# Optimization experiments

Measured on AMD Instinct MI355X. Metric: run time of the kernel, lower is better.

The kernel has to match this reference:

```python
import jax, jax.numpy as jnp
import numpy as np

B = 131072      # batch
G = 8           # number of groups
GS = 8          # features per group (n_features = G*GS = 64)
K = 8           # n_basis
O = 16          # kan_out_dim
TOT = G * O     # 128, GroupKANLayer output dim
R = 10          # n_rules
FIN = 20        # fuzzy_in_dim = max(2*n_rules, 8)
EPS_BN = 1e-5


def setup_inputs() -> dict:
    key = jax.random.key(0)
    ks = jax.random.split(key, 8)
    x = jax.random.normal(ks[0], (B, G * GS), dtype=jnp.float32)
    # per-group GaussianRBF params (one shared RBF per group, applied to each feature)
    rbf_centres = jnp.tile(jnp.linspace(-3.0, 3.0, K, dtype=jnp.float32)[None, :], (G, 1))
    rbf_log_widths = jnp.zeros((G, K), dtype=jnp.float32)
    rbf_weights = jax.random.normal(ks[1], (G, K), dtype=jnp.float32) * 0.1
    rbf_linear_w = jnp.ones((G,), dtype=jnp.float32)
    # group projections: kaiming normal fan_in (relu gain sqrt(2))
    proj_W = jax.random.normal(ks[2], (G, O, GS), dtype=jnp.float32) * np.sqrt(2.0 / GS)
    proj_b = jnp.zeros((G, O), dtype=jnp.float32)
    bn1_gamma = jnp.ones((TOT,), dtype=jnp.float32)
    bn1_beta = jnp.zeros((TOT,), dtype=jnp.float32)
    # fuzzy_proj linear (xavier uniform) TOT -> FIN
    a = np.sqrt(6.0 / (TOT + FIN))
    fp_W = jax.random.uniform(ks[3], (FIN, TOT), dtype=jnp.float32, minval=-a, maxval=a)
    fp_b = jnp.zeros((FIN,), dtype=jnp.float32)
    bn2_gamma = jnp.ones((FIN,), dtype=jnp.float32)
    bn2_beta = jnp.zeros((FIN,), dtype=jnp.float32)
    # IT2 fuzzy layer params
    fz_centres = jax.random.uniform(ks[4], (R, FIN), dtype=jnp.float32, minval=-1.0, maxval=1.0)
    fz_log_su = jnp.full((R, FIN), -0.7, dtype=jnp.float32)
    fz_log_sl = jnp.full((R, FIN), -1.2, dtype=jnp.float32)
    # sparse rule head
    head_W = jax.random.normal(ks[5], (1, R), dtype=jnp.float32) * 0.05
    head_b = jnp.zeros((1,), dtype=jnp.float32)
    return {
        'x': x, 'rbf_centres': rbf_centres, 'rbf_log_widths': rbf_log_widths,
        'rbf_weights': rbf_weights, 'rbf_linear_w': rbf_linear_w,
        'proj_W': proj_W, 'proj_b': proj_b,
        'bn1_gamma': bn1_gamma, 'bn1_beta': bn1_beta,
        'fp_W': fp_W, 'fp_b': fp_b, 'bn2_gamma': bn2_gamma, 'bn2_beta': bn2_beta,
        'fz_centres': fz_centres, 'fz_log_su': fz_log_su, 'fz_log_sl': fz_log_sl,
        'head_W': head_W, 'head_b': head_b,
    }


def _batchnorm(h, gamma, beta):
    # training-mode BatchNorm1d: normalize with batch mean / biased variance
    mu = h.mean(axis=0)
    var = h.var(axis=0)
    return (h - mu) * jax.lax.rsqrt(var + EPS_BN) * gamma + beta


def _forward(x, rbf_centres, rbf_log_widths, rbf_weights, rbf_linear_w,
             proj_W, proj_b, bn1_gamma, bn1_beta, fp_W, fp_b,
             bn2_gamma, bn2_beta, fz_centres, fz_log_su, fz_log_sl,
             head_W, head_b):
    b = x.shape[0]
    xg = x.reshape(b, G, GS)                               # groups are contiguous index slices
    sigma = jnp.exp(rbf_log_widths) + 1e-6                 # [G,K]
    # Gaussian RBF over all groups/features at once: [B,G,GS,K]
    rbf = jnp.exp(-0.5 * ((xg[..., None] - rbf_centres[:, None, :]) / sigma[:, None, :]) ** 2)
    act = rbf_linear_w[None, :, None] * xg + jnp.einsum('bgfk,gk->bgf', rbf, rbf_weights)
    proj = jnp.einsum('bgf,gof->bgo', act, proj_W) + proj_b  # grouped linear, [B,G,O]
    h = _batchnorm(proj.reshape(b, TOT), bn1_gamma, bn1_beta)
    # fuzzy_proj: Linear -> BN -> GELU (torch default GELU = exact erf form)
    z = _batchnorm(h @ fp_W.T + fp_b, bn2_gamma, bn2_beta)
    z = jax.nn.gelu(z, approximate=False)                    # [B,FIN]
    # IT2 fuzzy memberships
    su = jnp.exp(fz_log_su) + 1e-6                           # [R,FIN]
    sl = jnp.minimum(jnp.exp(fz_log_sl) + 1e-6, su * 0.9)
    diff = z[:, None, :] - fz_centres[None]                  # [B,R,FIN]
    upper = jnp.exp(-0.5 * (diff / su[None]) ** 2).mean(-1)  # [B,R]
    lower = jnp.exp(-0.5 * (diff / sl[None]) ** 2).mean(-1)
    firing = 0.5 * (upper + lower)
    return firing @ head_W.T + head_b                        # [B,1]


def reference(x, rbf_centres, rbf_log_widths, rbf_weights, rbf_linear_w,
              proj_W, proj_b, bn1_gamma, bn1_beta, fp_W, fp_b,
              bn2_gamma, bn2_beta, fz_centres, fz_log_su, fz_log_sl,
              head_W, head_b):
    return _forward(x, rbf_centres, rbf_log_widths, rbf_weights, rbf_linear_w,
                    proj_W, proj_b, bn1_gamma, bn1_beta, fp_W, fp_b,
                    bn2_gamma, bn2_beta, fz_centres, fz_log_su, fz_log_sl,
                    head_W, head_b)
```

## Files before the change

### kernel.cpp

```cpp
#include <hip/hip_runtime.h>
#include <hip/hip_fp16.h>
#include <math.h>

#define B_N 131072

#define WS_STAT1 0
#define ST1_SZ   (64 * 352)
#define WS_MT    22528
#define WS_C     23808
#define WS_STAT2 23840
#define WS_NH    26400
#define WS_ACTH  26816
#define WS_Z     (26816 + (size_t)B_N * 32)
#define WS_END   (WS_Z + (size_t)B_N * 20)

struct alignas(16) H8 { __half2 a, b, c, d; };

__device__ __forceinline__ float gelu_exact(float v) {
    return 0.5f * v * (1.0f + erff(v * 0.70710678118654752440f));
}

__global__ __launch_bounds__(256) void k_act_moments(
    const float* __restrict__ x, const float* __restrict__ cen,
    const float* __restrict__ lw, const float* __restrict__ rw,
    const float* __restrict__ linw, __half* __restrict__ act_h,
    float* __restrict__ stat1, int store)
{
    __shared__ float sAcc[4][8][44];
    const int t = threadIdx.x;
    const int g = t & 7;
    const int rl = t >> 3;

    float c_[8], nh_[8], w_[8];
#pragma unroll
    for (int k = 0; k < 8; ++k) {
        c_[k] = cen[g * 8 + k];
        float s = expf(lw[g * 8 + k]) + 1e-6f;
        nh_[k] = -0.5f / (s * s);
        w_[k] = rw[g * 8 + k];
    }
    const float lin = linw[g];
    const float c0 = c_[0], nh0 = nh_[0];
    const float delta = c_[1] - c_[0];

    bool uni = true;
#pragma unroll
    for (int k = 0; k < 8; ++k) {
        float ck = c0 + (float)k * delta;
        uni = uni && (fabsf(c_[k] - ck) <= 1e-5f * (1.0f + fabsf(ck)));
        uni = uni && (fabsf(nh_[k] - nh0) <= 1e-6f * fabsf(nh0));
    }
    const bool fast = (bool)__all((int)uni);

    float W_[8];
    float k1 = 0.0f;
    if (fast) {
        k1 = -2.0f * delta * nh0;
#pragma unroll
        for (int k = 0; k < 8; ++k) {
            float kd = (float)k * delta;
            W_[k] = w_[k] * __expf(nh0 * kd * kd);
        }
    }

    float sumA[8], P[36];
#pragma unroll
    for (int f = 0; f < 8; ++f) sumA[f] = 0.0f;
#pragma unroll
    for (int i = 0; i < 36; ++i) P[i] = 0.0f;

    if (fast) {
#pragma unroll 1
        for (int row = blockIdx.x * 32 + rl; row < B_N; row += gridDim.x * 32) {
            const float* xr = x + (size_t)row * 64 + g * 8;
            float4 v0 = *(const float4*)(xr);
            float4 v1 = *(const float4*)(xr + 4);
            float xv[8] = {v0.x, v0.y, v0.z, v0.w, v1.x, v1.y, v1.z, v1.w};
            float act[8];
#pragma unroll
            for (int f = 0; f < 8; ++f) {
                float v = xv[f];
                float dv = v - c0;
                float E0 = __expf(nh0 * dv * dv);
                float T  = __expf(k1 * dv);
                float poly = W_[7];
#pragma unroll
                for (int k = 6; k >= 0; --k) poly = poly * T + W_[k];
                act[f] = lin * v + E0 * poly;
            }
            if (store) {
                H8 h;
                h.a = __floats2half2_rn(act[0], act[1]);
                h.b = __floats2half2_rn(act[2], act[3]);
                h.c = __floats2half2_rn(act[4], act[5]);
                h.d = __floats2half2_rn(act[6], act[7]);
                *(H8*)(act_h + (size_t)row * 64 + g * 8) = h;
            }
            int idx = 0;
#pragma unroll
            for (int f = 0; f < 8; ++f) {
                sumA[f] += act[f];
#pragma unroll
                for (int f2 = 0; f2 <= f; ++f2) { P[idx] += act[f] * act[f2]; ++idx; }
            }
        }
    } else {
#pragma unroll 1
        for (int row = blockIdx.x * 32 + rl; row < B_N; row += gridDim.x * 32) {
            const float* xr = x + (size_t)row * 64 + g * 8;
            float4 v0 = *(const float4*)(xr);
            float4 v1 = *(const float4*)(xr + 4);
            float xv[8] = {v0.x, v0.y, v0.z, v0.w, v1.x, v1.y, v1.z, v1.w};
            float act[8];
#pragma unroll
            for (int f = 0; f < 8; ++f) {
                float v = xv[f];
                float a = lin * v;
#pragma unroll
                for (int k = 0; k < 8; ++k) {
                    float d = v - c_[k];
                    a += w_[k] * __expf(d * d * nh_[k]);
                }
                act[f] = a;
            }
            if (store) {
                H8 h;
                h.a = __floats2half2_rn(act[0], act[1]);
                h.b = __floats2half2_rn(act[2], act[3]);
                h.c = __floats2half2_rn(act[4], act[5]);
                h.d = __floats2half2_rn(act[6], act[7]);
                *(H8*)(act_h + (size_t)row * 64 + g * 8) = h;
            }
            int idx = 0;
#pragma unroll
            for (int f = 0; f < 8; ++f) {
                sumA[f] += act[f];
#pragma unroll
                for (int f2 = 0; f2 <= f; ++f2) { P[idx] += act[f] * act[f2]; ++idx; }
            }
        }
    }

#pragma unroll
    for (int off = 32; off >= 8; off >>= 1) {
#pragma unroll
        for (int f = 0; f < 8; ++f) sumA[f] += __shfl_down(sumA[f], off, 64);
#pragma unroll
        for (int i = 0; i < 36; ++i) P[i] += __shfl_down(P[i], off, 64);
    }
    const int wave = t >> 6, lane = t & 63;
    if (lane < 8) {
        float* dst = &sAcc[wave][lane][0];
#pragma unroll
        for (int f = 0; f < 8; ++f) dst[f] = sumA[f];
#pragma unroll
        for (int i = 0; i < 36; ++i) dst[8 + i] = P[i];
    }
    __syncthreads();
    for (int i = t; i < 352; i += 256) {
        int gg = i / 44, v = i % 44;
        float s = sAcc[0][gg][v] + sAcc[1][gg][v] + sAcc[2][gg][v] + sAcc[3][gg][v];
        atomicAdd(&stat1[(blockIdx.x & 63) * 352 + i], s);
    }
}

__global__ __launch_bounds__(256) void k_build(
    const float* __restrict__ stat1, const float* __restrict__ fpW,
    const float* __restrict__ fpb, const float* __restrict__ g1,
    const float* __restrict__ b1, const float* __restrict__ Wp,
    const float* __restrict__ pb, const float* __restrict__ lsu,
    const float* __restrict__ lsl,
    float* __restrict__ Mt, float* __restrict__ Cc, float* __restrict__ nh,
    float* __restrict__ stat2)
{
    __shared__ float Am[8][8];
    __shared__ float Sg[8][36];
    __shared__ float a_[128], bb_[128];
    const int t = threadIdx.x;
    for (int i = t; i < 352; i += 256) {
        float s = 0.0f;
        for (int st = 0; st < 64; ++st) s += stat1[st * 352 + i];
        float m = s * (1.0f / B_N);
        int g = i / 44, v = i % 44;
        if (v < 8) Am[g][v] = m; else Sg[g][v - 8] = m;
    }
    __syncthreads();
    if (t < 128) {
        const int g = t >> 4;
        float wv[8];
#pragma unroll
        for (int f = 0; f < 8; ++f) wv[f] = Wp[t * 8 + f];
        float dot = 0.0f;
#pragma unroll
        for (int f = 0; f < 8; ++f) dot += wv[f] * Am[g][f];
        const float pbv = pb[t];
        const float mu = pbv + dot;
        float e2 = pbv * pbv + 2.0f * pbv * dot;
        int idx = 0;
#pragma unroll
        for (int f = 0; f < 8; ++f)
#pragma unroll
            for (int f2 = 0; f2 <= f; ++f2) {
                float c2 = (f2 == f) ? 1.0f : 2.0f;
                e2 += c2 * wv[f] * wv[f2] * Sg[g][idx]; ++idx;
            }
        const float var = fmaxf(e2 - mu * mu, 0.0f);
        const float a = g1[t] * rsqrtf(var + 1e-5f);
        a_[t] = a;
        bb_[t] = b1[t] - mu * a;
    }
    __syncthreads();
    for (int i = t; i < 1280; i += 256) {
        int gf = i / 20, j = i % 20;
        int g = gf >> 3, f = gf & 7;
        float m = 0.0f;
        for (int o = 0; o < 16; ++o) {
            int c = g * 16 + o;
            m += fpW[j * 128 + c] * a_[c] * Wp[c * 8 + f];
        }
        Mt[i] = m;
    }
    if (t < 20) {
        float cj = fpb[t];
        for (int c = 0; c < 128; ++c)
            cj += fpW[t * 128 + c] * (a_[c] * pb[c] + bb_[c]);
        Cc[t] = cj;
    }
    for (int i = t; i < 200; i += 256) {
        float su = expf(lsu[i]) + 1e-6f;
        float sl = fminf(expf(lsl[i]) + 1e-6f, 0.9f * su);
        nh[i] = -0.5f / (su * su);
        nh[200 + i] = -0.5f / (sl * sl);
    }
    for (int i = t; i < 2560; i += 256) stat2[i] = 0.0f;
}

__global__ __launch_bounds__(256) void k_z(
    const __half* __restrict__ act_h, const float* __restrict__ Mt,
    const float* __restrict__ Cc, float* __restrict__ zout,
    float* __restrict__ stat2)
{
    __shared__ float sRed[4][40];
    const int t = threadIdx.x;
    const int row = blockIdx.x * 256 + t;

    float zp[20];
#pragma unroll
    for (int j = 0; j < 20; ++j) zp[j] = Cc[j];

#pragma unroll 1
    for (int g = 0; g < 8; ++g) {
        const H8 h = *(const H8*)(act_h + (size_t)row * 64 + g * 8);
        float2 f0 = __half22float2(h.a), f1 = __half22float2(h.b);
        float2 f2 = __half22float2(h.c), f3 = __half22float2(h.d);
        float a[8] = {f0.x, f0.y, f1.x, f1.y, f2.x, f2.y, f3.x, f3.y};
#pragma unroll
        for (int f = 0; f < 8; ++f) {
            const float* m = Mt + (g * 8 + f) * 20;
            float av = a[f];
#pragma unroll
            for (int j = 0; j < 20; ++j) zp[j] += av * m[j];
        }
    }

#pragma unroll
    for (int j = 0; j < 20; ++j) zout[(size_t)j * B_N + row] = zp[j];

    float s_[20], q_[20];
#pragma unroll
    for (int j = 0; j < 20; ++j) { s_[j] = zp[j]; q_[j] = zp[j] * zp[j]; }
#pragma unroll
    for (int off = 32; off >= 1; off >>= 1) {
#pragma unroll
        for (int j = 0; j < 20; ++j) {
            s_[j] += __shfl_down(s_[j], off, 64);
            q_[j] += __shfl_down(q_[j], off, 64);
        }
    }
    const int wave = t >> 6, lane = t & 63;
    if (lane == 0) {
#pragma unroll
        for (int j = 0; j < 20; ++j) { sRed[wave][j] = s_[j]; sRed[wave][20 + j] = q_[j]; }
    }
    __syncthreads();
    if (t < 40) {
        float v = sRed[0][t] + sRed[1][t] + sRed[2][t] + sRed[3][t];
        atomicAdd(&stat2[(blockIdx.x & 63) * 40 + t], v);
    }
}

__global__ __launch_bounds__(256) void k_zpre_stats(
    const float* __restrict__ x, const float* __restrict__ cen,
    const float* __restrict__ lw, const float* __restrict__ rw,
    const float* __restrict__ linw, const float* __restrict__ Mt,
    const float* __restrict__ Cc, float* __restrict__ zout,
    float* __restrict__ stat2)
{
    __shared__ __align__(16) float4 sRbf[64];
    __shared__ float sLin[8], sC[20];
    __shared__ __align__(16) float sMt[1280];
    __shared__ float sRed[4][40];
    const int t = threadIdx.x;
    if (t < 64) {
        float s = expf(lw[t]) + 1e-6f;
        sRbf[t] = make_float4(cen[t], rw[t], -0.5f / (s * s), 0.0f);
    }
    if (t < 8)  sLin[t] = linw[t];
    if (t < 20) sC[t] = Cc[t];
    for (int i = t; i < 1280; i += 256) sMt[i] = Mt[i];
    __syncthreads();
    const int row = blockIdx.x * 256 + t;
    const float* xr = x + (size_t)row * 64;
    float zp[20];
#pragma unroll
    for (int j = 0; j < 20; ++j) zp[j] = sC[j];
#pragma unroll 1
    for (int g = 0; g < 8; ++g) {
        float4 v0 = *(const float4*)(xr + g * 8);
        float4 v1 = *(const float4*)(xr + g * 8 + 4);
        float xv[8] = {v0.x, v0.y, v0.z, v0.w, v1.x, v1.y, v1.z, v1.w};
        float act[8];
        float lin = sLin[g];
#pragma unroll
        for (int f = 0; f < 8; ++f) act[f] = lin * xv[f];
#pragma unroll 1
        for (int k = 0; k < 8; ++k) {
            float4 p = sRbf[g * 8 + k];
#pragma unroll
            for (int f = 0; f < 8; ++f) {
                float d = xv[f] - p.x;
                act[f] += p.y * __expf(d * d * p.z);
            }
        }
#pragma unroll 1
        for (int f = 0; f < 8; ++f) {
            float av = act[f];
            const float4* m4 = (const float4*)(sMt + (g * 8 + f) * 20);
            float4 ma = m4[0], mb = m4[1], mc = m4[2], md = m4[3], me = m4[4];
            zp[0] += av * ma.x; zp[1] += av * ma.y; zp[2] += av * ma.z; zp[3] += av * ma.w;
            zp[4] += av * mb.x; zp[5] += av * mb.y; zp[6] += av * mb.z; zp[7] += av * mb.w;
            zp[8] += av * mc.x; zp[9] += av * mc.y; zp[10] += av * mc.z; zp[11] += av * mc.w;
            zp[12] += av * md.x; zp[13] += av * md.y; zp[14] += av * md.z; zp[15] += av * md.w;
            zp[16] += av * me.x; zp[17] += av * me.y; zp[18] += av * me.z; zp[19] += av * me.w;
        }
    }
#pragma unroll
    for (int j = 0; j < 20; ++j) zout[(size_t)j * B_N + row] = zp[j];
    float s_[20], q_[20];
#pragma unroll
    for (int j = 0; j < 20; ++j) { s_[j] = zp[j]; q_[j] = zp[j] * zp[j]; }
#pragma unroll
    for (int off = 32; off >= 1; off >>= 1) {
#pragma unroll
        for (int j = 0; j < 20; ++j) {
            s_[j] += __shfl_down(s_[j], off, 64);
            q_[j] += __shfl_down(q_[j], off, 64);
        }
    }
    const int wave = t >> 6, lane = t & 63;
    if (lane == 0) {
#pragma unroll
        for (int j = 0; j < 20; ++j) { sRed[wave][j] = s_[j]; sRed[wave][20 + j] = q_[j]; }
    }
    __syncthreads();
    if (t < 40) {
        float v = sRed[0][t] + sRed[1][t] + sRed[2][t] + sRed[3][t];
        atomicAdd(&stat2[(blockIdx.x & 63) * 40 + t], v);
    }
}

__global__ __launch_bounds__(256) void k_out(
    const float* __restrict__ zin, const float* __restrict__ stat2,
    const float* __restrict__ g2, const float* __restrict__ b2,
    const float* __restrict__ nh, const float* __restrict__ fzc,
    const float* __restrict__ hW, const float* __restrict__ hb,
    float* __restrict__ out)
{
    __shared__ float sT[40], sSc[20], sSh[20];
    const int t = threadIdx.x;
    if (t < 40) {
        float s = 0.0f;
        for (int st = 0; st < 64; ++st) s += stat2[st * 40 + t];
        sT[t] = s;
    }
    __syncthreads();
    if (t < 20) {
        float mu = sT[t] * (1.0f / B_N);
        float var = fmaxf(sT[20 + t] * (1.0f / B_N) - mu * mu, 0.0f);
        float sc = g2[t] * rsqrtf(var + 1e-5f);
        sSc[t] = sc;
        sSh[t] = b2[t] - mu * sc;
    }
    __syncthreads();

    const int row = blockIdx.x * 256 + t;
    float z[20];
#pragma unroll
    for (int j = 0; j < 20; ++j) {
        float v = zin[(size_t)j * B_N + row];
        z[j] = gelu_exact(sSc[j] * v + sSh[j]);
    }
    float acc = hb[0];
#pragma unroll 1
    for (int r = 0; r < 10; ++r) {
        float u = 0.0f, l = 0.0f;
#pragma unroll
        for (int j = 0; j < 20; ++j) {
            float cx = fzc[r * 20 + j];
            float pu = nh[r * 20 + j];
            float pl = nh[200 + r * 20 + j];
            float d = z[j] - cx;
            float dd = d * d;
            u += __expf(dd * pu);
            l += __expf(dd * pl);
        }
        acc += hW[r] * 0.025f * (u + l);
    }
    out[row] = acc;
}

extern "C" void kernel_launch(void* const* d_in, const int* in_sizes, int n_in,
                              void* d_out, int out_size, void* d_ws, size_t ws_size,
                              hipStream_t stream) {
    const float* x    = (const float*)d_in[0];
    const float* cen  = (const float*)d_in[1];
    const float* lw   = (const float*)d_in[2];
    const float* rw   = (const float*)d_in[3];
    const float* linw = (const float*)d_in[4];
    const float* Wp   = (const float*)d_in[5];
    const float* pb   = (const float*)d_in[6];
    const float* g1   = (const float*)d_in[7];
    const float* b1   = (const float*)d_in[8];
    const float* fpW  = (const float*)d_in[9];
    const float* fpb  = (const float*)d_in[10];
    const float* g2   = (const float*)d_in[11];
    const float* b2   = (const float*)d_in[12];
    const float* fzc  = (const float*)d_in[13];
    const float* lsu  = (const float*)d_in[14];
    const float* lsl  = (const float*)d_in[15];
    const float* hW   = (const float*)d_in[16];
    const float* hb   = (const float*)d_in[17];

    float* ws    = (float*)d_ws;
    float* stat1 = ws + WS_STAT1;
    float* Mt    = ws + WS_MT;
    float* Cc    = ws + WS_C;
    float* stat2 = ws + WS_STAT2;
    float* nh    = ws + WS_NH;
    __half* acth = (__half*)(ws + WS_ACTH);
    float* zbuf  = ws + WS_Z;
    float* outp  = (float*)d_out;

    const size_t needFull = WS_END * sizeof(float);
    const int mode = (ws_size >= needFull) ? 2 : 1;
    if (mode == 1) zbuf = ws + WS_ACTH;

    hipMemsetAsync(stat1, 0, (size_t)ST1_SZ * sizeof(float), stream);
    k_act_moments<<<1024, 256, 0, stream>>>(x, cen, lw, rw, linw, acth, stat1,
                                            mode == 2 ? 1 : 0);
    k_build<<<1, 256, 0, stream>>>(stat1, fpW, fpb, g1, b1, Wp, pb, lsu, lsl,
                                   Mt, Cc, nh, stat2);
    if (mode == 2) {
        k_z<<<512, 256, 0, stream>>>(acth, Mt, Cc, zbuf, stat2);
    } else {
        k_zpre_stats<<<512, 256, 0, stream>>>(x, cen, lw, rw, linw, Mt, Cc,
                                              zbuf, stat2);
    }
    k_out<<<512, 256, 0, stream>>>(zbuf, stat2, g2, b2, nh, fzc, hW, hb, outp);
}
```

Measured before the change: 162.2 us.

## Compute full 64x64 activation Gram to derive BN2 stats analytically, drop z pass

The stats kernel now accumulates the full 64x64 second-moment matrix of the RBF activations through a shared-memory tiled outer product, instead of only per-group moments. The build kernel uses it to compute the second batchnorm's mean and variance in closed form and folds the BN2 scale and shift into the projection matrix. That removes the intermediate z/activation buffers and the separate z-statistics kernel. The final kernel recomputes activations from x and applies GELU plus the fuzzy head directly, trading one full pass of reads and writes for extra atomics and a heavier single-block build step.

```diff
diff --git a/kernel.cpp b/kernel.cpp
--- a/kernel.cpp
+++ b/kernel.cpp
@@ -1,35 +1,32 @@
 #include <hip/hip_runtime.h>
-#include <hip/hip_fp16.h>
 #include <math.h>
 
 #define B_N 131072
-
-#define WS_STAT1 0
-#define ST1_SZ   (64 * 352)
-#define WS_MT    22528
-#define WS_C     23808
-#define WS_STAT2 23840
-#define WS_NH    26400
-#define WS_ACTH  26816
-#define WS_Z     (26816 + (size_t)B_N * 32)
-#define WS_END   (WS_Z + (size_t)B_N * 20)
-
-struct alignas(16) H8 { __half2 a, b, c, d; };
+#define NSTRIPE 16
+#define ST_STRIDE 4160
+#define WS_STAT 0
+#define ST_SZ   (NSTRIPE * ST_STRIDE)
+#define WS_MT2  66560
+#define WS_C2   67840
+#define WS_NH   67860
+#define WS_FT   68260
 
 __device__ __forceinline__ float gelu_exact(float v) {
     return 0.5f * v * (1.0f + erff(v * 0.70710678118654752440f));
 }
 
-__global__ __launch_bounds__(256) void k_act_moments(
+__global__ __launch_bounds__(256, 2) void k_stats(
     const float* __restrict__ x, const float* __restrict__ cen,
     const float* __restrict__ lw, const float* __restrict__ rw,
-    const float* __restrict__ linw, __half* __restrict__ act_h,
-    float* __restrict__ stat1, int store)
+    const float* __restrict__ linw, float* __restrict__ stat)
 {
-    __shared__ float sAcc[4][8][44];
-    const int t = threadIdx.x;
-    const int g = t & 7;
+    __shared__ float sAct[2][32][64];
+    __shared__ float sAcc[4][8][8];
+    const int t  = threadIdx.x;
+    const int g  = t & 7;
     const int rl = t >> 3;
+    const int gi = t >> 4;
+    const int gj = t & 15;
 
     float c_[8], nh_[8], w_[8];
 #pragma unroll
@@ -53,9 +50,9 @@
     const bool fast = (bool)__all((int)uni);
 
     float W_[8];
-    float k1 = 0.0f;
+    float k1c = 0.0f;
     if (fast) {
-        k1 = -2.0f * delta * nh0;
+        k1c = -2.0f * delta * nh0;
 #pragma unroll
         for (int k = 0; k < 8; ++k) {
             float kd = (float)k * delta;
@@ -63,55 +60,46 @@
         }
     }
 
-    float sumA[8], P[36];
+    float sumA[8];
 #pragma unroll
     for (int f = 0; f < 8; ++f) sumA[f] = 0.0f;
-#pragma unroll
-    for (int i = 0; i < 36; ++i) P[i] = 0.0f;
-
-    if (fast) {
+    float Ga[4][4];
+#pragma unroll
+    for (int a = 0; a < 4; ++a)
+#pragma unroll
+        for (int b = 0; b < 4; ++b) Ga[a][b] = 0.0f;
+
+    float4 pv0, pv1;
+    {
+        const float* xr = x + ((size_t)(blockIdx.x * 32 + rl)) * 64 + g * 8;
+        pv0 = *(const float4*)xr;
+        pv1 = *(const float4*)(xr + 4);
+    }
+
+    int p = 0;
 #pragma unroll 1
-        for (int row = blockIdx.x * 32 + rl; row < B_N; row += gridDim.x * 32) {
-            const float* xr = x + (size_t)row * 64 + g * 8;
-            float4 v0 = *(const float4*)(xr);
-            float4 v1 = *(const float4*)(xr + 4);
-            float xv[8] = {v0.x, v0.y, v0.z, v0.w, v1.x, v1.y, v1.z, v1.w};
-            float act[8];
+    for (int c = 0; c < 8; ++c) {
+        float xv[8] = {pv0.x, pv0.y, pv0.z, pv0.w, pv1.x, pv1.y, pv1.z, pv1.w};
+        if (c < 7) {
+            const float* xr =
+                x + ((size_t)(blockIdx.x * 32 + (c + 1) * 16384 + rl)) * 64 + g * 8;
+            pv0 = *(const float4*)xr;
+            pv1 = *(const float4*)(xr + 4);
+        }
+        float act[8];
+        if (fast) {
 #pragma unroll
             for (int f = 0; f < 8; ++f) {
                 float v = xv[f];
                 float dv = v - c0;
                 float E0 = __expf(nh0 * dv * dv);
-                float T  = __expf(k1 * dv);
+                float T  = __expf(k1c * dv);
                 float poly = W_[7];
 #pragma unroll
                 for (int k = 6; k >= 0; --k) poly = poly * T + W_[k];
                 act[f] = lin * v + E0 * poly;
             }
-            if (store) {
-                H8 h;
-                h.a = __floats2half2_rn(act[0], act[1]);
-                h.b = __floats2half2_rn(act[2], act[3]);
-                h.c = __floats2half2_rn(act[4], act[5]);
-                h.d = __floats2half2_rn(act[6], act[7]);
-                *(H8*)(act_h + (size_t)row * 64 + g * 8) = h;
-            }
-            int idx = 0;
-#pragma unroll
-            for (int f = 0; f < 8; ++f) {
-                sumA[f] += act[f];
-#pragma unroll
-                for (int f2 = 0; f2 <= f; ++f2) { P[idx] += act[f] * act[f2]; ++idx; }
-            }
-        }
-    } else {
-#pragma unroll 1
-        for (int row = blockIdx.x * 32 + rl; row < B_N; row += gridDim.x * 32) {
-            const float* xr = x + (size_t)row * 64 + g * 8;
-            float4 v0 = *(const float4*)(xr);
-            float4 v1 = *(const float4*)(xr + 4);
-            float xv[8] = {v0.x, v0.y, v0.z, v0.w, v1.x, v1.y, v1.z, v1.w};
-            float act[8];
+        } else {
 #pragma unroll
             for (int f = 0; f < 8; ++f) {
                 float v = xv[f];
@@ -123,68 +111,84 @@
                 }
                 act[f] = a;
             }
-            if (store) {
-                H8 h;
-                h.a = __floats2half2_rn(act[0], act[1]);
-                h.b = __floats2half2_rn(act[2], act[3]);
-                h.c = __floats2half2_rn(act[4], act[5]);
-                h.d = __floats2half2_rn(act[6], act[7]);
-                *(H8*)(act_h + (size_t)row * 64 + g * 8) = h;
-            }
-            int idx = 0;
-#pragma unroll
-            for (int f = 0; f < 8; ++f) {
-                sumA[f] += act[f];
-#pragma unroll
-                for (int f2 = 0; f2 <= f; ++f2) { P[idx] += act[f] * act[f2]; ++idx; }
-            }
-        }
-    }
-
-#pragma unroll
-    for (int off = 32; off >= 8; off >>= 1) {
+        }
+#pragma unroll
+        for (int f = 0; f < 8; ++f) sumA[f] += act[f];
+        *(float4*)&sAct[p][rl][g * 8]     = make_float4(act[0], act[1], act[2], act[3]);
+        *(float4*)&sAct[p][rl][g * 8 + 4] = make_float4(act[4], act[5], act[6], act[7]);
+        __syncthreads();
+        const float (*buf)[64] = sAct[p];
+#pragma unroll
+        for (int r = 0; r < 32; ++r) {
+            const float4 va = *(const float4*)&buf[r][gi * 4];
+            const float4 vb = *(const float4*)&buf[r][gj * 4];
+            Ga[0][0] += va.x * vb.x; Ga[0][1] += va.x * vb.y;
+            Ga[0][2] += va.x * vb.z; Ga[0][3] += va.x * vb.w;
+            Ga[1][0] += va.y * vb.x; Ga[1][1] += va.y * vb.y;
+            Ga[1][2] += va.y * vb.z; Ga[1][3] += va.y * vb.w;
+            Ga[2][0] += va.z * vb.x; Ga[2][1] += va.z * vb.y;
+            Ga[2][2] += va.z * vb.z; Ga[2][3] += va.z * vb.w;
+            Ga[3][0] += va.w * vb.x; Ga[3][1] += va.w * vb.y;
+            Ga[3][2] += va.w * vb.z; Ga[3][3] += va.w * vb.w;
+        }
+        p ^= 1;
+    }
+
+#pragma unroll
+    for (int off = 32; off >= 8; off >>= 1)
 #pragma unroll
         for (int f = 0; f < 8; ++f) sumA[f] += __shfl_down(sumA[f], off, 64);
-#pragma unroll
-        for (int i = 0; i < 36; ++i) P[i] += __shfl_down(P[i], off, 64);
-    }
     const int wave = t >> 6, lane = t & 63;
     if (lane < 8) {
-        float* dst = &sAcc[wave][lane][0];
-#pragma unroll
-        for (int f = 0; f < 8; ++f) dst[f] = sumA[f];
-#pragma unroll
-        for (int i = 0; i < 36; ++i) dst[8 + i] = P[i];
-    }
-    __syncthreads();
-    for (int i = t; i < 352; i += 256) {
-        int gg = i / 44, v = i % 44;
-        float s = sAcc[0][gg][v] + sAcc[1][gg][v] + sAcc[2][gg][v] + sAcc[3][gg][v];
-        atomicAdd(&stat1[(blockIdx.x & 63) * 352 + i], s);
-    }
+#pragma unroll
+        for (int f = 0; f < 8; ++f) sAcc[wave][lane][f] = sumA[f];
+    }
+    __syncthreads();
+    const int stripe = (blockIdx.x & (NSTRIPE - 1)) * ST_STRIDE;
+    if (t < 64) {
+        int gg = t >> 3, f = t & 7;
+        float s = sAcc[0][gg][f] + sAcc[1][gg][f] + sAcc[2][gg][f] + sAcc[3][gg][f];
+        atomicAdd(&stat[stripe + t], s);
+    }
+#pragma unroll
+    for (int a = 0; a < 4; ++a)
+#pragma unroll
+        for (int b = 0; b < 4; ++b)
+            atomicAdd(&stat[stripe + 64 + (gi * 4 + a) * 64 + (gj * 4 + b)], Ga[a][b]);
 }
 
 __global__ __launch_bounds__(256) void k_build(
-    const float* __restrict__ stat1, const float* __restrict__ fpW,
-    const float* __restrict__ fpb, const float* __restrict__ g1,
-    const float* __restrict__ b1, const float* __restrict__ Wp,
-    const float* __restrict__ pb, const float* __restrict__ lsu,
-    const float* __restrict__ lsl,
-    float* __restrict__ Mt, float* __restrict__ Cc, float* __restrict__ nh,
-    float* __restrict__ stat2)
+    const float* __restrict__ stat, const float* __restrict__ Wp,
+    const float* __restrict__ pb, const float* __restrict__ g1,
+    const float* __restrict__ b1, const float* __restrict__ fpW,
+    const float* __restrict__ fpb, const float* __restrict__ g2,
+    const float* __restrict__ b2, const float* __restrict__ lsu,
+    const float* __restrict__ lsl, const float* __restrict__ cen,
+    const float* __restrict__ lw, const float* __restrict__ rw,
+    const float* __restrict__ linw,
+    float* __restrict__ Mt2, float* __restrict__ C2,
+    float* __restrict__ nh, float* __restrict__ ftab)
 {
-    __shared__ float Am[8][8];
-    __shared__ float Sg[8][36];
-    __shared__ float a_[128], bb_[128];
+    __shared__ float sG[4096];
+    __shared__ float sAm[64];
+    __shared__ float sa[128], sbb[128];
+    __shared__ float sMt[1280];
+    __shared__ float sC[20];
+    __shared__ float sQ[20][8];
+    __shared__ float sDM[20];
+    __shared__ float sSc[20];
+    __shared__ int   sUni[8];
     const int t = threadIdx.x;
-    for (int i = t; i < 352; i += 256) {
+    const float invB = 1.0f / (float)B_N;
+
+    for (int i = t; i < ST_STRIDE; i += 256) {
         float s = 0.0f;
-        for (int st = 0; st < 64; ++st) s += stat1[st * 352 + i];
-        float m = s * (1.0f / B_N);
-        int g = i / 44, v = i % 44;
-        if (v < 8) Am[g][v] = m; else Sg[g][v - 8] = m;
-    }
-    __syncthreads();
+        for (int st = 0; st < NSTRIPE; ++st) s += stat[st * ST_STRIDE + i];
+        if (i < 64) sAm[i] = s * invB;
+        else        sG[i - 64] = s;
+    }
+    __syncthreads();
+
     if (t < 128) {
         const int g = t >> 4;
         float wv[8];
@@ -192,144 +196,190 @@
         for (int f = 0; f < 8; ++f) wv[f] = Wp[t * 8 + f];
         float dot = 0.0f;
 #pragma unroll
-        for (int f = 0; f < 8; ++f) dot += wv[f] * Am[g][f];
+        for (int f = 0; f < 8; ++f) dot += wv[f] * sAm[g * 8 + f];
         const float pbv = pb[t];
         const float mu = pbv + dot;
-        float e2 = pbv * pbv + 2.0f * pbv * dot;
-        int idx = 0;
-#pragma unroll
-        for (int f = 0; f < 8; ++f)
-#pragma unroll
-            for (int f2 = 0; f2 <= f; ++f2) {
-                float c2 = (f2 == f) ? 1.0f : 2.0f;
-                e2 += c2 * wv[f] * wv[f2] * Sg[g][idx]; ++idx;
-            }
-        const float var = fmaxf(e2 - mu * mu, 0.0f);
-        const float a = g1[t] * rsqrtf(var + 1e-5f);
-        a_[t] = a;
-        bb_[t] = b1[t] - mu * a;
-    }
-    __syncthreads();
+        float q = 0.0f;
+#pragma unroll
+        for (int f = 0; f < 8; ++f) {
+            float inner = 0.0f;
+#pragma unroll
+            for (int f2 = 0; f2 < 8; ++f2)
+                inner += wv[f2] * sG[(g * 8 + f) * 64 + (g * 8 + f2)];
+            q += wv[f] * inner;
+        }
+        float e2 = pbv * pbv + 2.0f * pbv * dot + q * invB;
+        float var = fmaxf(e2 - mu * mu, 0.0f);
+        float a = g1[t] * rsqrtf(var + 1e-5f);
+        sa[t] = a;
+        sbb[t] = b1[t] - mu * a;
+    }
+    __syncthreads();
+
     for (int i = t; i < 1280; i += 256) {
         int gf = i / 20, j = i % 20;
         int g = gf >> 3, f = gf & 7;
         float m = 0.0f;
         for (int o = 0; o < 16; ++o) {
             int c = g * 16 + o;
-            m += fpW[j * 128 + c] * a_[c] * Wp[c * 8 + f];
-        }
-        Mt[i] = m;
+            m += fpW[j * 128 + c] * sa[c] * Wp[c * 8 + f];
+        }
+        sMt[i] = m;
     }
     if (t < 20) {
         float cj = fpb[t];
         for (int c = 0; c < 128; ++c)
-            cj += fpW[t * 128 + c] * (a_[c] * pb[c] + bb_[c]);
-        Cc[t] = cj;
-    }
+            cj += fpW[t * 128 + c] * (sa[c] * pb[c] + sbb[c]);
+        sC[t] = cj;
+    }
+    __syncthreads();
+
+    if (t < 160) {
+        int j = t >> 3, pp = t & 7;
+        float qp = 0.0f;
+        for (int c = pp * 8; c < pp * 8 + 8; ++c) {
+            float inner = 0.0f;
+            for (int c2 = 0; c2 < 64; ++c2)
+                inner += sG[c * 64 + c2] * sMt[c2 * 20 + j];
+            qp += sMt[c * 20 + j] * inner;
+        }
+        sQ[j][pp] = qp;
+    } else if (t < 180) {
+        int j = t - 160;
+        float dm = 0.0f;
+        for (int c = 0; c < 64; ++c) dm += sMt[c * 20 + j] * sAm[c];
+        sDM[j] = dm;
+    }
+    __syncthreads();
+
+    if (t < 20) {
+        float q = 0.0f;
+#pragma unroll
+        for (int pp = 0; pp < 8; ++pp) q += sQ[t][pp];
+        q *= invB;
+        float Cj  = sC[t];
+        float dm  = sDM[t];
+        float mu2 = Cj + dm;
+        float Ez2 = Cj * Cj + 2.0f * Cj * dm + q;
+        float var = fmaxf(Ez2 - mu2 * mu2, 0.0f);
+        float sc = g2[t] * rsqrtf(var + 1e-5f);
+        sSc[t] = sc;
+        C2[t] = Cj * sc + (b2[t] - mu2 * sc);
+    }
+    __syncthreads();
+    for (int i = t; i < 1280; i += 256) Mt2[i] = sMt[i] * sSc[i % 20];
+
     for (int i = t; i < 200; i += 256) {
         float su = expf(lsu[i]) + 1e-6f;
         float sl = fminf(expf(lsl[i]) + 1e-6f, 0.9f * su);
-        nh[i] = -0.5f / (su * su);
+        nh[i]       = -0.5f / (su * su);
         nh[200 + i] = -0.5f / (sl * sl);
     }
-    for (int i = t; i < 2560; i += 256) stat2[i] = 0.0f;
+
+    if (t < 8) {
+        int gg = t;
+        float c0 = cen[gg * 8];
+        float delta = cen[gg * 8 + 1] - c0;
+        float s0 = expf(lw[gg * 8]) + 1e-6f;
+        float nh0 = -0.5f / (s0 * s0);
+        bool uni = true;
+        float Wk[8];
+#pragma unroll
+        for (int k = 0; k < 8; ++k) {
+            float ck = cen[gg * 8 + k];
+            float cke = c0 + (float)k * delta;
+            uni = uni && (fabsf(ck - cke) <= 1e-5f * (1.0f + fabsf(cke)));
+            float sk = expf(lw[gg * 8 + k]) + 1e-6f;
+            float nhk = -0.5f / (sk * sk);
+            uni = uni && (fabsf(nhk - nh0) <= 1e-6f * fabsf(nh0));
+            float kd = (float)k * delta;
+            Wk[k] = rw[gg * 8 + k] * __expf(nh0 * kd * kd);
+        }
+        ftab[gg * 12 + 0] = c0;
+        ftab[gg * 12 + 1] = -2.0f * delta * nh0;
+        ftab[gg * 12 + 2] = nh0;
+        ftab[gg * 12 + 3] = linw[gg];
+#pragma unroll
+        for (int k = 0; k < 8; ++k) ftab[gg * 12 + 4 + k] = Wk[k];
+        sUni[gg] = uni ? 1 : 0;
+    }
+    __syncthreads();
+    if (t == 0) {
+        int f = 1;
+        for (int gg = 0; gg < 8; ++gg) f &= sUni[gg];
+        ftab[96] = (float)f;
+    }
 }
 
-__global__ __launch_bounds__(256) void k_z(
-    const __half* __restrict__ act_h, const float* __restrict__ Mt,
-    const float* __restrict__ Cc, float* __restrict__ zout,
-    float* __restrict__ stat2)
-{
-    __shared__ float sRed[4][40];
-    const int t = threadIdx.x;
-    const int row = blockIdx.x * 256 + t;
-
-    float zp[20];
-#pragma unroll
-    for (int j = 0; j < 20; ++j) zp[j] = Cc[j];
-
-#pragma unroll 1
-    for (int g = 0; g < 8; ++g) {
-        const H8 h = *(const H8*)(act_h + (size_t)row * 64 + g * 8);
-        float2 f0 = __half22float2(h.a), f1 = __half22float2(h.b);
-        float2 f2 = __half22float2(h.c), f3 = __half22float2(h.d);
-        float a[8] = {f0.x, f0.y, f1.x, f1.y, f2.x, f2.y, f3.x, f3.y};
-#pragma unroll
-        for (int f = 0; f < 8; ++f) {
-            const float* m = Mt + (g * 8 + f) * 20;
-            float av = a[f];
-#pragma unroll
-            for (int j = 0; j < 20; ++j) zp[j] += av * m[j];
-        }
-    }
-
-#pragma unroll
-    for (int j = 0; j < 20; ++j) zout[(size_t)j * B_N + row] = zp[j];
-
-    float s_[20], q_[20];
-#pragma unroll
-    for (int j = 0; j < 20; ++j) { s_[j] = zp[j]; q_[j] = zp[j] * zp[j]; }
-#pragma unroll
-    for (int off = 32; off >= 1; off >>= 1) {
-#pragma unroll
-        for (int j = 0; j < 20; ++j) {
-            s_[j] += __shfl_down(s_[j], off, 64);
-            q_[j] += __shfl_down(q_[j], off, 64);
-        }
-    }
-    const int wave = t >> 6, lane = t & 63;
-    if (lane == 0) {
-#pragma unroll
-        for (int j = 0; j < 20; ++j) { sRed[wave][j] = s_[j]; sRed[wave][20 + j] = q_[j]; }
-    }
-    __syncthreads();
-    if (t < 40) {
-        float v = sRed[0][t] + sRed[1][t] + sRed[2][t] + sRed[3][t];
-        atomicAdd(&stat2[(blockIdx.x & 63) * 40 + t], v);
-    }
-}
-
-__global__ __launch_bounds__(256) void k_zpre_stats(
+__global__ __launch_bounds__(256, 2) void k_out(
     const float* __restrict__ x, const float* __restrict__ cen,
     const float* __restrict__ lw, const float* __restrict__ rw,
-    const float* __restrict__ linw, const float* __restrict__ Mt,
-    const float* __restrict__ Cc, float* __restrict__ zout,
-    float* __restrict__ stat2)
+    const float* __restrict__ linw, const float* __restrict__ Mt2,
+    const float* __restrict__ C2, const float* __restrict__ nh,
+    const float* __restrict__ fzc, const float* __restrict__ hW,
+    const float* __restrict__ hb, const float* __restrict__ ftab,
+    float* __restrict__ out)
 {
+    __shared__ __align__(16) float sMt[1280];
+    __shared__ float sC[20];
+    __shared__ float sTab[97];
     __shared__ __align__(16) float4 sRbf[64];
-    __shared__ float sLin[8], sC[20];
-    __shared__ __align__(16) float sMt[1280];
-    __shared__ float sRed[4][40];
+    __shared__ float sLin[8];
     const int t = threadIdx.x;
+    for (int i = t; i < 1280; i += 256) sMt[i] = Mt2[i];
+    if (t < 20) sC[t] = C2[t];
+    if (t < 97) sTab[t] = ftab[t];
     if (t < 64) {
         float s = expf(lw[t]) + 1e-6f;
         sRbf[t] = make_float4(cen[t], rw[t], -0.5f / (s * s), 0.0f);
     }
-    if (t < 8)  sLin[t] = linw[t];
-    if (t < 20) sC[t] = Cc[t];
-    for (int i = t; i < 1280; i += 256) sMt[i] = Mt[i];
-    __syncthreads();
+    if (t < 8) sLin[t] = linw[t];
+    __syncthreads();
+    const bool fast = (sTab[96] > 0.5f);
+
     const int row = blockIdx.x * 256 + t;
     const float* xr = x + (size_t)row * 64;
     float zp[20];
 #pragma unroll
     for (int j = 0; j < 20; ++j) zp[j] = sC[j];
+
 #pragma unroll 1
     for (int g = 0; g < 8; ++g) {
         float4 v0 = *(const float4*)(xr + g * 8);
         float4 v1 = *(const float4*)(xr + g * 8 + 4);
         float xv[8] = {v0.x, v0.y, v0.z, v0.w, v1.x, v1.y, v1.z, v1.w};
         float act[8];
-        float lin = sLin[g];
-#pragma unroll
-        for (int f = 0; f < 8; ++f) act[f] = lin * xv[f];
+        if (fast) {
+            const float c0  = sTab[g * 12 + 0];
+            const float k1c = sTab[g * 12 + 1];
+            const float nh0 = sTab[g * 12 + 2];
+            const float lin = sTab[g * 12 + 3];
+            float Wk[8];
+#pragma unroll
+            for (int k = 0; k < 8; ++k) Wk[k] = sTab[g * 12 + 4 + k];
+#pragma unroll
+            for (int f = 0; f < 8; ++f) {
+                float v = xv[f];
+                float dv = v - c0;
+                float E0 = __expf(nh0 * dv * dv);
+                float T  = __expf(k1c * dv);
+                float poly = Wk[7];
+#pragma unroll
+                for (int k = 6; k >= 0; --k) poly = poly * T + Wk[k];
+                act[f] = lin * v + E0 * poly;
+            }
+        } else {
+            float lin = sLin[g];
+#pragma unroll
+            for (int f = 0; f < 8; ++f) act[f] = lin * xv[f];
 #pragma unroll 1
-        for (int k = 0; k < 8; ++k) {
-            float4 p = sRbf[g * 8 + k];
-#pragma unroll
-            for (int f = 0; f < 8; ++f) {
-                float d = xv[f] - p.x;
-                act[f] += p.y * __expf(d * d * p.z);
+            for (int k = 0; k < 8; ++k) {
+                float4 pr = sRbf[g * 8 + k];
+#pragma unroll
+                for (int f = 0; f < 8; ++f) {
+                    float d = xv[f] - pr.x;
+                    act[f] += pr.y * __expf(d * d * pr.z);
+                }
             }
         }
 #pragma unroll 1
@@ -344,62 +394,10 @@
             zp[16] += av * me.x; zp[17] += av * me.y; zp[18] += av * me.z; zp[19] += av * me.w;
         }
     }
-#pragma unroll
-    for (int j = 0; j < 20; ++j) zout[(size_t)j * B_N + row] = zp[j];
-    float s_[20], q_[20];
-#pragma unroll
-    for (int j = 0; j < 20; ++j) { s_[j] = zp[j]; q_[j] = zp[j] * zp[j]; }
-#pragma unroll
-    for (int off = 32; off >= 1; off >>= 1) {
-#pragma unroll
-        for (int j = 0; j < 20; ++j) {
-            s_[j] += __shfl_down(s_[j], off, 64);
-            q_[j] += __shfl_down(q_[j], off, 64);
-        }
-    }
-    const int wave = t >> 6, lane = t & 63;
-    if (lane == 0) {
-#pragma unroll
-        for (int j = 0; j < 20; ++j) { sRed[wave][j] = s_[j]; sRed[wave][20 + j] = q_[j]; }
-    }
-    __syncthreads();
-    if (t < 40) {
-        float v = sRed[0][t] + sRed[1][t] + sRed[2][t] + sRed[3][t];
-        atomicAdd(&stat2[(blockIdx.x & 63) * 40 + t], v);
-    }
-}
-
-__global__ __launch_bounds__(256) void k_out(
-    const float* __restrict__ zin, const float* __restrict__ stat2,
-    const float* __restrict__ g2, const float* __restrict__ b2,
-    const float* __restrict__ nh, const float* __restrict__ fzc,
-    const float* __restrict__ hW, const float* __restrict__ hb,
-    float* __restrict__ out)
-{
-    __shared__ float sT[40], sSc[20], sSh[20];
-    const int t = threadIdx.x;
-    if (t < 40) {
-        float s = 0.0f;
-        for (int st = 0; st < 64; ++st) s += stat2[st * 40 + t];
-        sT[t] = s;
-    }
-    __syncthreads();
-    if (t < 20) {
-        float mu = sT[t] * (1.0f / B_N);
-        float var = fmaxf(sT[20 + t] * (1.0f / B_N) - mu * mu, 0.0f);
-        float sc = g2[t] * rsqrtf(var + 1e-5f);
-        sSc[t] = sc;
-        sSh[t] = b2[t] - mu * sc;
-    }
-    __syncthreads();
-
-    const int row = blockIdx.x * 256 + t;
-    float z[20];
-#pragma unroll
-    for (int j = 0; j < 20; ++j) {
-        float v = zin[(size_t)j * B_N + row];
-        z[j] = gelu_exact(sSc[j] * v + sSh[j]);
-    }
+
+#pragma unroll
+    for (int j = 0; j < 20; ++j) zp[j] = gelu_exact(zp[j]);
+
     float acc = hb[0];
 #pragma unroll 1
     for (int r = 0; r < 10; ++r) {
@@ -409,7 +407,7 @@
             float cx = fzc[r * 20 + j];
             float pu = nh[r * 20 + j];
             float pl = nh[200 + r * 20 + j];
-            float d = z[j] - cx;
+            float d = zp[j] - cx;
             float dd = d * d;
             u += __expf(dd * pu);
             l += __expf(dd * pl);
@@ -441,30 +439,19 @@
     const float* hW   = (const float*)d_in[16];
     const float* hb   = (const float*)d_in[17];
 
-    float* ws    = (float*)d_ws;
-    float* stat1 = ws + WS_STAT1;
-    float* Mt    = ws + WS_MT;
-    float* Cc    = ws + WS_C;
-    float* stat2 = ws + WS_STAT2;
-    float* nh    = ws + WS_NH;
-    __half* acth = (__half*)(ws + WS_ACTH);
-    float* zbuf  = ws + WS_Z;
-    float* outp  = (float*)d_out;
-
-    const size_t needFull = WS_END * sizeof(float);
-    const int mode = (ws_size >= needFull) ? 2 : 1;
-    if (mode == 1) zbuf = ws + WS_ACTH;
-
-    hipMemsetAsync(stat1, 0, (size_t)ST1_SZ * sizeof(float), stream);
-    k_act_moments<<<1024, 256, 0, stream>>>(x, cen, lw, rw, linw, acth, stat1,
-                                            mode == 2 ? 1 : 0);
-    k_build<<<1, 256, 0, stream>>>(stat1, fpW, fpb, g1, b1, Wp, pb, lsu, lsl,
-                                   Mt, Cc, nh, stat2);
-    if (mode == 2) {
-        k_z<<<512, 256, 0, stream>>>(acth, Mt, Cc, zbuf, stat2);
-    } else {
-        k_zpre_stats<<<512, 256, 0, stream>>>(x, cen, lw, rw, linw, Mt, Cc,
-                                              zbuf, stat2);
-    }
-    k_out<<<512, 256, 0, stream>>>(zbuf, stat2, g2, b2, nh, fzc, hW, hb, outp);
+    float* ws   = (float*)d_ws;
+    float* stat = ws + WS_STAT;
+    float* Mt2  = ws + WS_MT2;
+    float* C2   = ws + WS_C2;
+    float* nh   = ws + WS_NH;
+    float* ftab = ws + WS_FT;
+    float* outp = (float*)d_out;
+
+    hipMemsetAsync(stat, 0, (size_t)ST_SZ * sizeof(float), stream);
+    k_stats<<<512, 256, 0, stream>>>(x, cen, lw, rw, linw, stat);
+    k_build<<<1, 256, 0, stream>>>(stat, Wp, pb, g1, b1, fpW, fpb, g2, b2,
+                                   lsu, lsl, cen, lw, rw, linw,
+                                   Mt2, C2, nh, ftab);
+    k_out<<<512, 256, 0, stream>>>(x, cen, lw, rw, linw, Mt2, C2, nh, fzc,
+                                   hW, hb, ftab, outp);
 }
```

Measured after the change: 206.3 us. 1.27x slower.

## Replace atomic stripe accumulation with per-block partials and drop memset

Applied to the files above, without the earlier changes.

Each block now writes its reduced moment statistics to its own slot in a partials buffer instead of atomically adding into 64 shared stripes. This removes the hipMemsetAsync launch and the zeroing of stat2 in k_build. The consumer kernels now reduce all 512 per-block partials themselves. k_moments drops from 1024 to 512 blocks, and the low-workspace fallback path (k_zpre_stats) is removed, so the code now assumes the workspace is always large enough. The extra cost is a longer serial reduction inside the single-block k_build.

```diff
diff --git a/kernel.cpp b/kernel.cpp
--- a/kernel.cpp
+++ b/kernel.cpp
@@ -3,16 +3,16 @@
 #include <math.h>
 
 #define B_N 131072
-
-#define WS_STAT1 0
-#define ST1_SZ   (64 * 352)
-#define WS_MT    22528
-#define WS_C     23808
-#define WS_STAT2 23840
-#define WS_NH    26400
-#define WS_ACTH  26816
-#define WS_Z     (26816 + (size_t)B_N * 32)
-#define WS_END   (WS_Z + (size_t)B_N * 20)
+#define NSTRIPE1 512
+#define NSTRIPE2 512
+
+#define WS_P1   0
+#define WS_P2   (NSTRIPE1 * 352)
+#define WS_MT   (WS_P2 + NSTRIPE2 * 40)
+#define WS_C    (WS_MT + 1280)
+#define WS_NH   (WS_C + 20)
+#define WS_ACTH (WS_NH + 400)
+#define WS_Z    (WS_ACTH + (size_t)B_N * 32)
 
 struct alignas(16) H8 { __half2 a, b, c, d; };
 
@@ -20,11 +20,11 @@
     return 0.5f * v * (1.0f + erff(v * 0.70710678118654752440f));
 }
 
-__global__ __launch_bounds__(256) void k_act_moments(
+__global__ __launch_bounds__(256) void k_moments(
     const float* __restrict__ x, const float* __restrict__ cen,
     const float* __restrict__ lw, const float* __restrict__ rw,
     const float* __restrict__ linw, __half* __restrict__ act_h,
-    float* __restrict__ stat1, int store)
+    float* __restrict__ part1)
 {
     __shared__ float sAcc[4][8][44];
     const int t = threadIdx.x;
@@ -88,14 +88,12 @@
                 for (int k = 6; k >= 0; --k) poly = poly * T + W_[k];
                 act[f] = lin * v + E0 * poly;
             }
-            if (store) {
-                H8 h;
-                h.a = __floats2half2_rn(act[0], act[1]);
-                h.b = __floats2half2_rn(act[2], act[3]);
-                h.c = __floats2half2_rn(act[4], act[5]);
-                h.d = __floats2half2_rn(act[6], act[7]);
-                *(H8*)(act_h + (size_t)row * 64 + g * 8) = h;
-            }
+            H8 h;
+            h.a = __floats2half2_rn(act[0], act[1]);
+            h.b = __floats2half2_rn(act[2], act[3]);
+            h.c = __floats2half2_rn(act[4], act[5]);
+            h.d = __floats2half2_rn(act[6], act[7]);
+            *(H8*)(act_h + (size_t)row * 64 + g * 8) = h;
             int idx = 0;
 #pragma unroll
             for (int f = 0; f < 8; ++f) {
@@ -123,14 +121,12 @@
                 }
                 act[f] = a;
             }
-            if (store) {
-                H8 h;
-                h.a = __floats2half2_rn(act[0], act[1]);
-                h.b = __floats2half2_rn(act[2], act[3]);
-                h.c = __floats2half2_rn(act[4], act[5]);
-                h.d = __floats2half2_rn(act[6], act[7]);
-                *(H8*)(act_h + (size_t)row * 64 + g * 8) = h;
-            }
+            H8 h;
+            h.a = __floats2half2_rn(act[0], act[1]);
+            h.b = __floats2half2_rn(act[2], act[3]);
+            h.c = __floats2half2_rn(act[4], act[5]);
+            h.d = __floats2half2_rn(act[6], act[7]);
+            *(H8*)(act_h + (size_t)row * 64 + g * 8) = h;
             int idx = 0;
 #pragma unroll
             for (int f = 0; f < 8; ++f) {
@@ -157,30 +153,36 @@
         for (int i = 0; i < 36; ++i) dst[8 + i] = P[i];
     }
     __syncthreads();
+    float* S = part1 + (size_t)blockIdx.x * 352;
     for (int i = t; i < 352; i += 256) {
         int gg = i / 44, v = i % 44;
-        float s = sAcc[0][gg][v] + sAcc[1][gg][v] + sAcc[2][gg][v] + sAcc[3][gg][v];
-        atomicAdd(&stat1[(blockIdx.x & 63) * 352 + i], s);
+        S[i] = sAcc[0][gg][v] + sAcc[1][gg][v] + sAcc[2][gg][v] + sAcc[3][gg][v];
     }
 }
 
 __global__ __launch_bounds__(256) void k_build(
-    const float* __restrict__ stat1, const float* __restrict__ fpW,
+    const float* __restrict__ part1, const float* __restrict__ fpW,
     const float* __restrict__ fpb, const float* __restrict__ g1,
     const float* __restrict__ b1, const float* __restrict__ Wp,
     const float* __restrict__ pb, const float* __restrict__ lsu,
     const float* __restrict__ lsl,
-    float* __restrict__ Mt, float* __restrict__ Cc, float* __restrict__ nh,
-    float* __restrict__ stat2)
+    float* __restrict__ Mt, float* __restrict__ Cc, float* __restrict__ nh)
 {
     __shared__ float Am[8][8];
     __shared__ float Sg[8][36];
     __shared__ float a_[128], bb_[128];
     const int t = threadIdx.x;
     for (int i = t; i < 352; i += 256) {
-        float s = 0.0f;
-        for (int st = 0; st < 64; ++st) s += stat1[st * 352 + i];
-        float m = s * (1.0f / B_N);
+        const float* p = part1 + i;
+        float s0 = 0.0f, s1 = 0.0f, s2 = 0.0f, s3 = 0.0f;
+#pragma unroll 4
+        for (int st = 0; st < NSTRIPE1; st += 4) {
+            s0 += p[(st    ) * 352];
+            s1 += p[(st + 1) * 352];
+            s2 += p[(st + 2) * 352];
+            s3 += p[(st + 3) * 352];
+        }
+        float m = ((s0 + s1) + (s2 + s3)) * (1.0f / B_N);
         int g = i / 44, v = i % 44;
         if (v < 8) Am[g][v] = m; else Sg[g][v - 8] = m;
     }
@@ -232,13 +234,12 @@
         nh[i] = -0.5f / (su * su);
         nh[200 + i] = -0.5f / (sl * sl);
     }
-    for (int i = t; i < 2560; i += 256) stat2[i] = 0.0f;
 }
 
 __global__ __launch_bounds__(256) void k_z(
     const __half* __restrict__ act_h, const float* __restrict__ Mt,
     const float* __restrict__ Cc, float* __restrict__ zout,
-    float* __restrict__ stat2)
+    float* __restrict__ part2)
 {
     __shared__ float sRed[4][40];
     const int t = threadIdx.x;
@@ -283,106 +284,30 @@
         for (int j = 0; j < 20; ++j) { sRed[wave][j] = s_[j]; sRed[wave][20 + j] = q_[j]; }
     }
     __syncthreads();
-    if (t < 40) {
-        float v = sRed[0][t] + sRed[1][t] + sRed[2][t] + sRed[3][t];
-        atomicAdd(&stat2[(blockIdx.x & 63) * 40 + t], v);
-    }
-}
-
-__global__ __launch_bounds__(256) void k_zpre_stats(
-    const float* __restrict__ x, const float* __restrict__ cen,
-    const float* __restrict__ lw, const float* __restrict__ rw,
-    const float* __restrict__ linw, const float* __restrict__ Mt,
-    const float* __restrict__ Cc, float* __restrict__ zout,
-    float* __restrict__ stat2)
-{
-    __shared__ __align__(16) float4 sRbf[64];
-    __shared__ float sLin[8], sC[20];
-    __shared__ __align__(16) float sMt[1280];
-    __shared__ float sRed[4][40];
-    const int t = threadIdx.x;
-    if (t < 64) {
-        float s = expf(lw[t]) + 1e-6f;
-        sRbf[t] = make_float4(cen[t], rw[t], -0.5f / (s * s), 0.0f);
-    }
-    if (t < 8)  sLin[t] = linw[t];
-    if (t < 20) sC[t] = Cc[t];
-    for (int i = t; i < 1280; i += 256) sMt[i] = Mt[i];
-    __syncthreads();
-    const int row = blockIdx.x * 256 + t;
-    const float* xr = x + (size_t)row * 64;
-    float zp[20];
-#pragma unroll
-    for (int j = 0; j < 20; ++j) zp[j] = sC[j];
-#pragma unroll 1
-    for (int g = 0; g < 8; ++g) {
-        float4 v0 = *(const float4*)(xr + g * 8);
-        float4 v1 = *(const float4*)(xr + g * 8 + 4);
-        float xv[8] = {v0.x, v0.y, v0.z, v0.w, v1.x, v1.y, v1.z, v1.w};
-        float act[8];
-        float lin = sLin[g];
-#pragma unroll
-        for (int f = 0; f < 8; ++f) act[f] = lin * xv[f];
-#pragma unroll 1
-        for (int k = 0; k < 8; ++k) {
-            float4 p = sRbf[g * 8 + k];
-#pragma unroll
-            for (int f = 0; f < 8; ++f) {
-                float d = xv[f] - p.x;
-                act[f] += p.y * __expf(d * d * p.z);
-            }
-        }
-#pragma unroll 1
-        for (int f = 0; f < 8; ++f) {
-            float av = act[f];
-            const float4* m4 = (const float4*)(sMt + (g * 8 + f) * 20);
-            float4 ma = m4[0], mb = m4[1], mc = m4[2], md = m4[3], me = m4[4];
-            zp[0] += av * ma.x; zp[1] += av * ma.y; zp[2] += av * ma.z; zp[3] += av * ma.w;
-            zp[4] += av * mb.x; zp[5] += av * mb.y; zp[6] += av * mb.z; zp[7] += av * mb.w;
-            zp[8] += av * mc.x; zp[9] += av * mc.y; zp[10] += av * mc.z; zp[11] += av * mc.w;
-            zp[12] += av * md.x; zp[13] += av * md.y; zp[14] += av * md.z; zp[15] += av * md.w;
-            zp[16] += av * me.x; zp[17] += av * me.y; zp[18] += av * me.z; zp[19] += av * me.w;
-        }
-    }
-#pragma unroll
-    for (int j = 0; j < 20; ++j) zout[(size_t)j * B_N + row] = zp[j];
-    float s_[20], q_[20];
-#pragma unroll
-    for (int j = 0; j < 20; ++j) { s_[j] = zp[j]; q_[j] = zp[j] * zp[j]; }
-#pragma unroll
-    for (int off = 32; off >= 1; off >>= 1) {
-#pragma unroll
-        for (int j = 0; j < 20; ++j) {
-            s_[j] += __shfl_down(s_[j], off, 64);
-            q_[j] += __shfl_down(q_[j], off, 64);
-        }
-    }
-    const int wave = t >> 6, lane = t & 63;
-    if (lane == 0) {
-#pragma unroll
-        for (int j = 0; j < 20; ++j) { sRed[wave][j] = s_[j]; sRed[wave][20 + j] = q_[j]; }
-    }
-    __syncthreads();
-    if (t < 40) {
-        float v = sRed[0][t] + sRed[1][t] + sRed[2][t] + sRed[3][t];
-        atomicAdd(&stat2[(blockIdx.x & 63) * 40 + t], v);
-    }
+    if (t < 40)
+        part2[(size_t)blockIdx.x * 40 + t] =
+            sRed[0][t] + sRed[1][t] + sRed[2][t] + sRed[3][t];
 }
 
 __global__ __launch_bounds__(256) void k_out(
-    const float* __restrict__ zin, const float* __restrict__ stat2,
+    const float* __restrict__ zin, const float* __restrict__ part2,
     const float* __restrict__ g2, const float* __restrict__ b2,
     const float* __restrict__ nh, const float* __restrict__ fzc,
     const float* __restrict__ hW, const float* __restrict__ hb,
     float* __restrict__ out)
 {
+    __shared__ float sT6[6][40];
     __shared__ float sT[40], sSc[20], sSh[20];
     const int t = threadIdx.x;
-    if (t < 40) {
+    if (t < 240) {
+        const int p = t / 40, e = t - p * 40;
         float s = 0.0f;
-        for (int st = 0; st < 64; ++st) s += stat2[st * 40 + t];
-        sT[t] = s;
-    }
+        for (int st = p; st < NSTRIPE2; st += 6) s += part2[(size_t)st * 40 + e];
+        sT6[p][e] = s;
+    }
+    __syncthreads();
+    if (t < 40)
+        sT[t] = sT6[0][t] + sT6[1][t] + sT6[2][t] + sT6[3][t] + sT6[4][t] + sT6[5][t];
     __syncthreads();
     if (t < 20) {
         float mu = sT[t] * (1.0f / B_N);
@@ -442,29 +367,18 @@
     const float* hb   = (const float*)d_in[17];
 
     float* ws    = (float*)d_ws;
-    float* stat1 = ws + WS_STAT1;
+    float* part1 = ws + WS_P1;
+    float* part2 = ws + WS_P2;
     float* Mt    = ws + WS_MT;
     float* Cc    = ws + WS_C;
-    float* stat2 = ws + WS_STAT2;
     float* nh    = ws + WS_NH;
     __half* acth = (__half*)(ws + WS_ACTH);
     float* zbuf  = ws + WS_Z;
     float* outp  = (float*)d_out;
 
-    const size_t needFull = WS_END * sizeof(float);
-    const int mode = (ws_size >= needFull) ? 2 : 1;
-    if (mode == 1) zbuf = ws + WS_ACTH;
-
-    hipMemsetAsync(stat1, 0, (size_t)ST1_SZ * sizeof(float), stream);
-    k_act_moments<<<1024, 256, 0, stream>>>(x, cen, lw, rw, linw, acth, stat1,
-                                            mode == 2 ? 1 : 0);
-    k_build<<<1, 256, 0, stream>>>(stat1, fpW, fpb, g1, b1, Wp, pb, lsu, lsl,
-                                   Mt, Cc, nh, stat2);
-    if (mode == 2) {
-        k_z<<<512, 256, 0, stream>>>(acth, Mt, Cc, zbuf, stat2);
-    } else {
-        k_zpre_stats<<<512, 256, 0, stream>>>(x, cen, lw, rw, linw, Mt, Cc,
-                                              zbuf, stat2);
-    }
-    k_out<<<512, 256, 0, stream>>>(zbuf, stat2, g2, b2, nh, fzc, hW, hb, outp);
-}
+    k_moments<<<NSTRIPE1, 256, 0, stream>>>(x, cen, lw, rw, linw, acth, part1);
+    k_build<<<1, 256, 0, stream>>>(part1, fpW, fpb, g1, b1, Wp, pb, lsu, lsl,
+                                   Mt, Cc, nh);
+    k_z<<<NSTRIPE2, 256, 0, stream>>>(acth, Mt, Cc, zbuf, part2);
+    k_out<<<512, 256, 0, stream>>>(zbuf, part2, g2, b2, nh, fzc, hW, hb, outp);
+}
```

Result: slower. 197.3 us (+21.6%).
